# Kernel tuning notes

Measured on AMD Instinct MI355X. Metric: run time of the kernel, lower is better.

## Reference

```python
import jax, jax.numpy as jnp
import numpy as np

QB = 127.0  # act_bits=8 -> 2**(8-1)-1
EPS = 1e-5


def _ste(x, q):
    # straight-through estimator: forward = q, backward = identity
    return x + jax.lax.stop_gradient(q - x)


def bitlinear(x, W, b):
    """BitNet-b1.58 linear: ternary weights (per-tensor mean-abs scale),
    8-bit per-token absmax activations, dequantized matmul + bias."""
    w_scale = jnp.clip(jnp.mean(jnp.abs(W)), EPS, None)
    Wq = _ste(W, jnp.clip(jnp.round(W / w_scale), -1.0, 1.0) * w_scale)  # ternary * scale
    x_scale = jnp.clip(jnp.max(jnp.abs(x), axis=-1, keepdims=True), EPS, None)
    xq = _ste(x, jnp.clip(jnp.round(x * (QB / x_scale)), -QB - 1.0, QB) * (x_scale / QB))
    # x: [B, N, d_in], W: [d_out, d_in] -> [B, N, d_out]
    return jnp.einsum('bnd,hd->bnh', xq, Wq) + b


def setup_inputs() -> dict:
    key = jax.random.key(0)
    k0, k1, k2 = jax.random.split(key, 3)
    B, N, D = 8, 4096, 1024
    H = int(D * 4.0)
    x = jax.random.normal(k0, (B, N, D), dtype=jnp.float32)
    W1 = jax.random.normal(k1, (H, D), dtype=jnp.float32) * 0.02
    b1 = jnp.zeros((H,), dtype=jnp.float32)
    W2 = jax.random.normal(k2, (D, H), dtype=jnp.float32) * 0.02
    b2 = jnp.zeros((D,), dtype=jnp.float32)
    return {"x": x, "W1": W1, "b1": b1, "W2": W2, "b2": b2}


def reference(x, W1, b1, W2, b2):
    h = bitlinear(x, W1, b1)                 # [B, N, H]
    h = jax.nn.gelu(h, approximate=False)    # torch nn.GELU default = exact erf
    # dropout with p=0.0 is identity
    return bitlinear(h, W2, b2)              # [B, N, D]
```

## Files before the change

### kernel.cpp

```cpp
#include <hip/hip_runtime.h>
#include <hip/hip_bf16.h>
#include <math.h>


typedef int int32x4 __attribute__((ext_vector_type(4)));

typedef const void __attribute__((address_space(1))) gv_t;
typedef void __attribute__((address_space(3))) lv_t;

__device__ __forceinline__ void gload_lds16(const signed char* g,
                                            signed char* l) {
  __builtin_amdgcn_global_load_lds((gv_t*)g, (lv_t*)l, 16, 0, 0);
}

__device__ __forceinline__ float gelu_erf(float v) {
  return 0.5f * v * (1.0f + erff(v * 0.70710678118654752440f));
}

__device__ __forceinline__ void store_gt(float* p, float v) { *p = v; }
__device__ __forceinline__ void store_gt(__hip_bfloat16* p, float v) {
  unsigned u = __float_as_uint(v);
  u += 0x7fffu + ((u >> 16) & 1u);
  *(unsigned short*)p = (unsigned short)(u >> 16);
}

__device__ __forceinline__ void load4v(const float* p, float v[4]) {
  const float4 t = *(const float4*)p;
  v[0] = t.x; v[1] = t.y; v[2] = t.z; v[3] = t.w;
}
__device__ __forceinline__ void load4v(const __hip_bfloat16* p, float v[4]) {
  const ushort4 t = *(const ushort4*)p;
  v[0] = __uint_as_float((unsigned)t.x << 16);
  v[1] = __uint_as_float((unsigned)t.y << 16);
  v[2] = __uint_as_float((unsigned)t.z << 16);
  v[3] = __uint_as_float((unsigned)t.w << 16);
}

__global__ __launch_bounds__(256) void absmean_partial(
    const float* __restrict__ W, double* __restrict__ part) {
  const int tid = threadIdx.x;
  const long base = (long)blockIdx.x * 8192;
  double s = 0.0;
#pragma unroll
  for (int c = 0; c < 8; ++c) {
    const float4 v = *(const float4*)&W[base + c * 1024 + tid * 4];
    s += (double)fabsf(v.x) + (double)fabsf(v.y) +
         (double)fabsf(v.z) + (double)fabsf(v.w);
  }
  __shared__ double sm[256];
  sm[tid] = s; __syncthreads();
  for (int off = 128; off; off >>= 1) {
    if (tid < off) sm[tid] += sm[tid + off];
    __syncthreads();
  }
  if (tid == 0) part[blockIdx.x] = sm[0];
}

__global__ __launch_bounds__(256) void absmean_final(
    const double* __restrict__ part, double* __restrict__ out, double n) {
  const int tid = threadIdx.x;
  __shared__ double sm[256];
  sm[tid] = part[tid] + part[tid + 256];
  __syncthreads();
  for (int off = 128; off; off >>= 1) {
    if (tid < off) sm[tid] += sm[tid + off];
    __syncthreads();
  }
  if (tid == 0) out[0] = fmax(sm[0] / n, 1e-5);
}

__global__ __launch_bounds__(256) void quant_w(
    const float* __restrict__ W, const double* __restrict__ wsP,
    signed char* __restrict__ Wq) {
  const double ws = *wsP;
  const long i = ((long)blockIdx.x * 256 + threadIdx.x) * 4;
  const float4 v = *(const float4*)&W[i];
  const float vv[4] = {v.x, v.y, v.z, v.w};
  int pack = 0;
#pragma unroll
  for (int q = 0; q < 4; ++q) {
    double r = rint((double)vv[q] / ws);
    r = fmin(fmax(r, -1.0), 1.0);
    pack |= (((int)r) & 0xff) << (8 * q);
  }
  *(int*)&Wq[i] = pack;
}

template <int L, bool GELU, typename GT>
__global__ __launch_bounds__(256) void quant_rows(
    const GT* __restrict__ X, signed char* __restrict__ Xq,
    float* __restrict__ dsc) {
  constexpr int CH = L / 1024;
  const long row = blockIdx.x;
  const int tid = threadIdx.x;
  const GT* xr = X + row * (long)L;
  float v[CH][4];
  float m = 0.f;
#pragma unroll
  for (int c = 0; c < CH; ++c) {
    load4v(xr + c * 1024 + tid * 4, v[c]);
#pragma unroll
    for (int q = 0; q < 4; ++q) {
      if (GELU) v[c][q] = gelu_erf(v[c][q]);
      m = fmaxf(m, fabsf(v[c][q]));
    }
  }
#pragma unroll
  for (int off = 32; off; off >>= 1) m = fmaxf(m, __shfl_down(m, off, 64));
  __shared__ float wmx[4];
  if ((tid & 63) == 0) wmx[tid >> 6] = m;
  __syncthreads();
  float ms = fmaxf(fmaxf(wmx[0], wmx[1]), fmaxf(wmx[2], wmx[3]));
  ms = fmaxf(ms, 1e-5f);
  const double inv = 127.0 / (double)ms;
#pragma unroll
  for (int c = 0; c < CH; ++c) {
    int pack = 0;
#pragma unroll
    for (int q = 0; q < 4; ++q) {
      double r = rint((double)v[c][q] * inv);
      r = fmin(fmax(r, -128.0), 127.0);
      pack |= (((int)r) & 0xff) << (8 * q);
    }
    *(int*)&Xq[row * (long)L + c * 1024 + tid * 4] = pack;
  }
  if (tid == 0) dsc[row] = (float)((double)ms / 127.0);
}

template <typename GT>
__global__ __launch_bounds__(512, 4) void gemm_i8_2b(
    const signed char* __restrict__ A, const signed char* __restrict__ Bm,
    const float* __restrict__ dA, const double* __restrict__ wsB,
    const float* __restrict__ bias, GT* __restrict__ C,
    int K, int Ncol, int nx) {
  __shared__ signed char LDS[49152];
  const int tid = threadIdx.x;
  const int lane = tid & 63;
  const int wave = tid >> 6;
  const int wm = wave >> 2;
  const int wn = wave & 3;

  const int cpx = gridDim.x >> 3;
  const int wg = ((int)blockIdx.x & 7) * cpx + ((int)blockIdx.x >> 3);
  const long rowBase = (long)(wg / nx) * 128;
  const long colBase = (long)(wg % nx) * 256;
  const int NT = K >> 6;

  const int sr = tid >> 2;
  const int sc = ((tid & 3) << 4) ^ ((sr & 3) << 4);
  const signed char* gAr = A + (rowBase + sr) * (long)K + sc;
  const signed char* gBr = Bm + (colBase + sr) * (long)K + sc;
  const signed char* gBr2 = gBr + 128L * K;
  const int da = tid << 4;

  auto STAGE = [&](int t) {
    const long ko = (long)t << 6;
    gload_lds16(gAr + ko, &LDS[((t & 1) << 13) + da]);
    gload_lds16(gBr + ko, &LDS[16384 + ((t & 1) << 14) + da]);
    gload_lds16(gBr2 + ko, &LDS[16384 + ((t & 1) << 14) + 8192 + da]);
  };

  const int rl = lane & 15;
  const int axor = (((lane >> 4) ^ (rl & 3)) << 4);
  const int aoff = (wm * 64 + rl) * 64 + axor;
  const int boff = (wn * 64 + rl) * 64 + axor;

  int32x4 acc[4][4] = {};
  int32x4 af[4], bf[4];

  STAGE(0);

  for (int t = 0; t < NT; ++t) {
    if (t + 1 < NT) {
      STAGE(t + 1);
      asm volatile("s_waitcnt vmcnt(3)" ::: "memory");
    } else {
      asm volatile("s_waitcnt vmcnt(0)" ::: "memory");
    }
    __builtin_amdgcn_s_barrier();

    const signed char* At = &LDS[(t & 1) << 13];
    const signed char* Bt = &LDS[16384 + ((t & 1) << 14)];
#pragma unroll
    for (int mi = 0; mi < 4; ++mi)
      af[mi] = *(const int32x4*)(At + aoff + mi * 1024);
#pragma unroll
    for (int nj = 0; nj < 4; ++nj)
      bf[nj] = *(const int32x4*)(Bt + boff + nj * 1024);

    __builtin_amdgcn_s_setprio(1);
#pragma unroll
    for (int mi = 0; mi < 4; ++mi)
#pragma unroll
      for (int nj = 0; nj < 4; ++nj)
        acc[mi][nj] = __builtin_amdgcn_mfma_i32_16x16x64_i8(
            af[mi], bf[nj], acc[mi][nj], 0, 0, 0);
    __builtin_amdgcn_s_setprio(0);

    asm volatile("s_waitcnt lgkmcnt(0)" ::: "memory");
    __builtin_amdgcn_s_barrier();
  }

  const double wsd = *wsB;
  const int rq = (lane >> 4) << 2;
  float bv[4];
#pragma unroll
  for (int nj = 0; nj < 4; ++nj)
    bv[nj] = bias[colBase + wn * 64 + nj * 16 + rl];
#pragma unroll
  for (int mi = 0; mi < 4; ++mi) {
#pragma unroll
    for (int r = 0; r < 4; ++r) {
      const long row = rowBase + wm * 64 + mi * 16 + rq + r;
      const float sc2 = (float)((double)dA[row] * wsd);
      GT* crow = C + row * (long)Ncol + colBase + wn * 64 + rl;
#pragma unroll
      for (int nj = 0; nj < 4; ++nj)
        store_gt(&crow[nj * 16], (float)acc[mi][nj][r] * sc2 + bv[nj]);
    }
  }
}

extern "C" void kernel_launch(void* const* d_in, const int* in_sizes, int n_in,
                              void* d_out, int out_size, void* d_ws,
                              size_t ws_size, hipStream_t stream) {
  const float* x  = (const float*)d_in[0];
  const float* W1 = (const float*)d_in[1];
  const float* b1 = (const float*)d_in[2];
  const float* W2 = (const float*)d_in[3];
  const float* b2 = (const float*)d_in[4];
  const int D = in_sizes[4];
  const int H = in_sizes[2];
  const long M = (long)in_sizes[0] / D;
  float* out = (float*)d_out;

  if (D != 1024 || H != 4096 || (M % 128) != 0) return;

  char* wsp = (char*)d_ws;
  size_t off = 0;
  auto alloc = [&](size_t bytes) {
    void* p = wsp + off;
    off = (off + bytes + 255) & ~(size_t)255;
    return p;
  };
  signed char* wq1 = (signed char*)alloc((size_t)H * D);
  signed char* wq2 = (signed char*)alloc((size_t)D * H);
  signed char* xq  = (signed char*)alloc((size_t)M * D);
  signed char* gq  = (signed char*)alloc((size_t)M * H);
  float* dx = (float*)alloc((size_t)M * 4);
  float* dg = (float*)alloc((size_t)M * 4);
  double* part = (double*)alloc(512 * 8);
  double* ws1 = (double*)alloc(8);
  double* ws2 = (double*)alloc(8);
  __hip_bfloat16* h = (__hip_bfloat16*)alloc((size_t)M * H * 2);
  if (off > ws_size) return;

  const long nW = (long)H * D;
  absmean_partial<<<nW / 8192, 256, 0, stream>>>(W1, part);
  absmean_final<<<1, 256, 0, stream>>>(part, ws1, (double)nW);
  absmean_partial<<<nW / 8192, 256, 0, stream>>>(W2, part);
  absmean_final<<<1, 256, 0, stream>>>(part, ws2, (double)nW);
  quant_w<<<nW / 1024, 256, 0, stream>>>(W1, ws1, wq1);
  quant_w<<<nW / 1024, 256, 0, stream>>>(W2, ws2, wq2);
  quant_rows<1024, false, float><<<M, 256, 0, stream>>>(x, xq, dx);

  const int g1 = (int)(M / 128) * (H / 256);
  const int g2 = (int)(M / 128) * (D / 256);
  gemm_i8_2b<__hip_bfloat16><<<g1, 512, 0, stream>>>(
      xq, wq1, dx, ws1, b1, h, D, H, H / 256);
  quant_rows<4096, true, __hip_bfloat16><<<M, 256, 0, stream>>>(h, gq, dg);
  gemm_i8_2b<float><<<g2, 512, 0, stream>>>(
      gq, wq2, dg, ws2, b2, out, H, D, D / 256);
}
```

Before: 499.1 us.

## Load B operand directly from global into registers, stage only A via LDS

```diff
diff --git a/kernel.cpp b/kernel.cpp
--- a/kernel.cpp
+++ b/kernel.cpp
@@ -128,12 +128,12 @@
 }
 
 template <typename GT>
-__global__ __launch_bounds__(512, 4) void gemm_i8_2b(
+__global__ __launch_bounds__(512, 4) void gemm_i8_bl2(
     const signed char* __restrict__ A, const signed char* __restrict__ Bm,
     const float* __restrict__ dA, const double* __restrict__ wsB,
     const float* __restrict__ bias, GT* __restrict__ C,
     int K, int Ncol, int nx) {
-  __shared__ signed char LDS[49152];
+  __shared__ signed char LDS[16384];
   const int tid = threadIdx.x;
   const int lane = tid & 63;
   const int wave = tid >> 6;
@@ -147,46 +147,44 @@
   const int NT = K >> 6;
 
   const int sr = tid >> 2;
-  const int sc = ((tid & 3) << 4) ^ ((sr & 3) << 4);
-  const signed char* gAr = A + (rowBase + sr) * (long)K + sc;
-  const signed char* gBr = Bm + (colBase + sr) * (long)K + sc;
-  const signed char* gBr2 = gBr + 128L * K;
+  const int scc = (((tid & 3) ^ ((tid >> 3) & 3)) << 4);
+  const signed char* gAr = A + (rowBase + sr) * (long)K + scc;
   const int da = tid << 4;
 
-  auto STAGE = [&](int t) {
-    const long ko = (long)t << 6;
-    gload_lds16(gAr + ko, &LDS[((t & 1) << 13) + da]);
-    gload_lds16(gBr + ko, &LDS[16384 + ((t & 1) << 14) + da]);
-    gload_lds16(gBr2 + ko, &LDS[16384 + ((t & 1) << 14) + 8192 + da]);
+  auto STAGE_A = [&](int t) {
+    gload_lds16(gAr + ((long)t << 6), &LDS[((t & 1) << 13) + da]);
   };
 
   const int rl = lane & 15;
-  const int axor = (((lane >> 4) ^ (rl & 3)) << 4);
-  const int aoff = (wm * 64 + rl) * 64 + axor;
-  const int boff = (wn * 64 + rl) * 64 + axor;
+  const signed char* Bq = Bm + (colBase + wn * 64) * (long)K +
+                          (long)rl * K + (((lane >> 4) & 3) << 4);
+  auto LOADB = [&](int32x4 (&bfd)[4], int t) {
+    const signed char* bp = Bq + ((long)t << 6);
+#pragma unroll
+    for (int nj = 0; nj < 4; ++nj)
+      bfd[nj] = *(const int32x4*)(bp + (long)nj * 16 * K);
+  };
+
+  const int aswz = ((lane >> 4) ^ ((rl >> 1) & 3)) << 4;
+  const int aoff = (wm * 64 + rl) * 64 + aswz;
 
   int32x4 acc[4][4] = {};
-  int32x4 af[4], bf[4];
-
-  STAGE(0);
-
-  for (int t = 0; t < NT; ++t) {
-    if (t + 1 < NT) {
-      STAGE(t + 1);
-      asm volatile("s_waitcnt vmcnt(3)" ::: "memory");
-    } else {
-      asm volatile("s_waitcnt vmcnt(0)" ::: "memory");
-    }
+  int32x4 af[4], bfE[4], bfO[4];
+
+  STAGE_A(0);
+  LOADB(bfE, 0);
+  LOADB(bfO, 1);
+
+  auto TILE = [&](int t, int32x4 (&bfc)[4]) {
+    if (t + 1 < NT) STAGE_A(t + 1);
+    if (t < NT - 1) asm volatile("s_waitcnt vmcnt(5)" ::: "memory");
+    else            asm volatile("s_waitcnt vmcnt(0)" ::: "memory");
     __builtin_amdgcn_s_barrier();
 
     const signed char* At = &LDS[(t & 1) << 13];
-    const signed char* Bt = &LDS[16384 + ((t & 1) << 14)];
 #pragma unroll
     for (int mi = 0; mi < 4; ++mi)
       af[mi] = *(const int32x4*)(At + aoff + mi * 1024);
-#pragma unroll
-    for (int nj = 0; nj < 4; ++nj)
-      bf[nj] = *(const int32x4*)(Bt + boff + nj * 1024);
 
     __builtin_amdgcn_s_setprio(1);
 #pragma unroll
@@ -194,11 +192,18 @@
 #pragma unroll
       for (int nj = 0; nj < 4; ++nj)
         acc[mi][nj] = __builtin_amdgcn_mfma_i32_16x16x64_i8(
-            af[mi], bf[nj], acc[mi][nj], 0, 0, 0);
+            af[mi], bfc[nj], acc[mi][nj], 0, 0, 0);
     __builtin_amdgcn_s_setprio(0);
+
+    if (t + 2 < NT) LOADB(bfc, t + 2);
 
     asm volatile("s_waitcnt lgkmcnt(0)" ::: "memory");
     __builtin_amdgcn_s_barrier();
+  };
+
+  for (int t = 0; t < NT; t += 2) {
+    TILE(t, bfE);
+    TILE(t + 1, bfO);
   }
 
   const double wsd = *wsB;
@@ -266,9 +271,9 @@
 
   const int g1 = (int)(M / 128) * (H / 256);
   const int g2 = (int)(M / 128) * (D / 256);
-  gemm_i8_2b<__hip_bfloat16><<<g1, 512, 0, stream>>>(
+  gemm_i8_bl2<__hip_bfloat16><<<g1, 512, 0, stream>>>(
       xq, wq1, dx, ws1, b1, h, D, H, H / 256);
   quant_rows<4096, true, __hip_bfloat16><<<M, 256, 0, stream>>>(h, gq, dg);
-  gemm_i8_2b<float><<<g2, 512, 0, stream>>>(
+  gemm_i8_bl2<float><<<g2, 512, 0, stream>>>(
       gq, wq2, dg, ws2, b2, out, H, D, D / 256);
 }
```

Result: slower. 868.3 us (+74.0%).
